# Kernel optimization log

Measured on AMD Instinct MI355X. Metric: run time of the kernel, lower is better.

The kernel has to match this reference:

```python
import jax, jax.numpy as jnp
import numpy as np

COUNT_PRIOR_LOG_ODDS = -2.0  # frozen value of exponential_decay(**cfg.OBJ_PRES_COUNT_LOG_PRIOR)
EPS = 1e-9                   # safe_log epsilon
B, H, W = 1024, 16, 16


def setup_inputs() -> dict:
    key = jax.random.key(0)
    k1, k2 = jax.random.split(key)
    z_pres = jax.random.uniform(k1, (B, 1, H, W), dtype=jnp.float32)
    z_pres_prob = jax.random.uniform(k2, (B, 1, H, W), dtype=jnp.float32)
    return {"z_pres": z_pres, "z_pres_prob": z_pres_prob}


def _safe_log(x):
    return jnp.log(x + EPS)


def reference(z_pres, z_pres_prob):
    b, _, h, w = z_pres.shape
    hw = h * w
    s = hw + 1  # count support size

    count_support = jnp.arange(s, dtype=jnp.float32)  # [S]
    p = 1.0 / (jnp.exp(jnp.float32(-COUNT_PRIOR_LOG_ODDS)) + 1.0)
    cd0 = (1.0 - p) * p ** count_support
    cd0 = cd0 / cd0.sum()
    cd0 = jnp.broadcast_to(cd0[None, :], (b, s))      # count_distribution [B, S]
    csf0 = jnp.zeros((b, 1), jnp.float32)             # count_so_far [B, 1]

    # flatten grid in row-major (h, w) order to scan axis: [HW, B, 1]
    probs = z_pres_prob.reshape(b, 1, hw).transpose(2, 0, 1)
    pres = z_pres.reshape(b, 1, hw).transpose(2, 0, 1)
    steps = jnp.arange(hw, dtype=jnp.float32)

    def step(carry, xs):
        cd, csf = carry                 # [B, S], [B, 1]
        prob, zp, i = xs                # [B, 1], [B, 1], scalar
        denom = hw - i
        # P(z=1 | C, z_prev): clamp(count_support - count_so_far, 0, HW - i) / (HW - i)
        p_z_given = jnp.clip(count_support[None, :] - csf, 0.0, denom) / denom  # [B, S]
        p_z = jnp.sum(cd * p_z_given, axis=1, keepdims=True)                    # [B, 1] (the bmm)
        kl = (prob * (_safe_log(prob) - _safe_log(p_z))
              + (1.0 - prob) * (_safe_log(1.0 - prob) - _safe_log(1.0 - p_z)))
        sample = jnp.round(zp)                                                  # [B, 1]
        mult = sample * p_z_given + (1.0 - sample) * (1.0 - p_z_given)          # [B, S]
        cd1 = mult * cd
        norm = jnp.clip(jnp.sum(cd1, axis=1, keepdims=True), 1e-6, None)
        return (cd1 / norm, csf + sample), kl

    (_, _), kls = jax.lax.scan(step, (cd0, csf0), (probs, pres, steps))
    # kls: [HW, B, 1] -> obj_kl [B, 1, H, W]
    return kls.transpose(1, 2, 0).reshape(b, 1, h, w)
```

## Files before the change

kernel.cpp:

```cpp
#include <hip/hip_runtime.h>
#include <math.h>

#define HW 256
#define MINNORM 1.17549435e-38f


template <int CTRL>
__device__ __forceinline__ float dpp_sra(float x) {
    int s = __builtin_amdgcn_update_dpp(0, __builtin_bit_cast(int, x),
                                        CTRL, 0xf, 0xf, true);
    return x + __builtin_bit_cast(float, s);
}

__device__ __forceinline__ float rdlane(float x, int l) {
    return __builtin_bit_cast(float,
        __builtin_amdgcn_readlane(__builtin_bit_cast(int, x), l));
}

__device__ __forceinline__ void wave_total2(float x, float y,
                                            float& sx, float& sy) {
    x = dpp_sra<0x111>(x);  y = dpp_sra<0x111>(y);
    x = dpp_sra<0x112>(x);  y = dpp_sra<0x112>(y);
    x = dpp_sra<0x114>(x);  y = dpp_sra<0x114>(y);
    x = dpp_sra<0x118>(x);  y = dpp_sra<0x118>(y);
    const float a0 = rdlane(x, 15), b0 = rdlane(y, 15);
    const float a1 = rdlane(x, 31), b1 = rdlane(y, 31);
    const float a2 = rdlane(x, 47), b2 = rdlane(y, 47);
    sx = (a0 + a1) + a2;
    sy = (b0 + b1) + b2;
}

__global__ void __launch_bounds__(64, 1)
spair_count_kl(const float* __restrict__ z_pres,
               const float* __restrict__ z_prob,
               float* __restrict__ out) {
    float tok;
    asm volatile("s_setreg_imm32_b32 hwreg(HW_REG_MODE, 4, 2), 0\n\t"
                 "v_mov_b32 %0, 0" : "=v"(tok));

    const int lane = threadIdx.x;
    const int b = blockIdx.x;

    const float e2f = (float)exp(2.0);
    const float pf  = (float)(1.0 / ((double)e2f + 1.0));
    const double pd = (double)pf;
    const double l2p = log2(pd);
    float cd = 0.0f;
    if (lane <= 41) {
        const double powj = exp2((double)lane * l2p);
        float v = (float)((1.0 - pd) * powj);
        cd = (v < MINNORM) ? 0.0f : v;
    }
    {
        float s = cd;
#pragma unroll
        for (int off = 32; off > 0; off >>= 1) s += __shfl_xor(s, off, 64);
        cd = cd / s;
    }
    cd += tok;
    const float jf = (float)lane;
    float csf = tok;

    const float it0 = 1.0f / (float)(HW - lane);
    const float it1 = 1.0f / (float)(HW - 64 - lane);
    const float it2 = 1.0f / (float)(HW - 128 - lane);
    const float it3 = 1.0f / (float)(HW - 192 - lane);

    const float* presb = z_pres + (size_t)b * HW;
    const float* probb = z_prob + (size_t)b * HW;
    float* outb = out + (size_t)b * HW;

    bool dead = false;

#pragma unroll 1
    for (int k = 0; k < 4; ++k) {
        const float myprob = probb[k * 64 + lane];
        const float mypres = presb[k * 64 + lane];
        const unsigned long long smask = __ballot(rintf(mypres) != 0.0f);
        float my_pz = 0.0f;
        const float itk = (k == 0) ? it0 : (k == 1) ? it1 : (k == 2) ? it2 : it3;

        if (!dead) {
#pragma unroll 1
            for (int blk = 0; blk < 4; ++blk) {
                float p2 = 1.0f;
#pragma unroll
                for (int u = 0; u < 16; ++u) {
                    const int ii = blk * 16 + u;
                    const int i = k * 64 + ii;
                    const float fden = (float)(HW - i);
                    const float inv = rdlane(itk, ii);
                    const bool s1 = ((smask >> ii) & 1ULL) != 0ULL;

                    const float t = fminf(fmaxf(jf - csf, 0.0f), fden);
                    const float pg = (t == fden) ? 1.0f : t * inv;
                    const float mult = s1 ? pg : (1.0f - pg);

                    const float prodm = cd * mult;
                    const float p1 = cd * pg;
                    float p1s;
                    wave_total2(prodm, p1, p2, p1s);
                    const float norm = fmaxf(p2, 1e-6f);
                    const float invn = __builtin_amdgcn_rcpf(norm);
                    cd = prodm * invn;
                    csf += s1 ? 1.0f : 0.0f;

                    const float pz = s1 ? p2 : p1s;
                    my_pz = (ii == lane) ? pz : my_pz;
                }
                if (p2 == 0.0f) { dead = true; break; }
            }
        }

        const float prob = myprob;
        const float pz = my_pz;
        const float kl = prob * (logf(prob + 1e-9f) - logf(pz + 1e-9f))
                       + (1.0f - prob) * (logf((1.0f - prob) + 1e-9f)
                                        - logf((1.0f - pz) + 1e-9f));
        outb[k * 64 + lane] = kl;
    }
}

extern "C" void kernel_launch(void* const* d_in, const int* in_sizes, int n_in,
                              void* d_out, int out_size, void* d_ws, size_t ws_size,
                              hipStream_t stream) {
    const float* z_pres = (const float*)d_in[0];
    const float* z_prob = (const float*)d_in[1];
    float* out = (float*)d_out;
    const int nbatch = in_sizes[0] / HW;
    spair_count_kl<<<dim3(nbatch), dim3(64), 0, stream>>>(z_pres, z_prob, out);
}
```

Baseline: 69.35 us.

## Fuse two scan steps per wave reduction round to halve serial reductions

Processes scan steps in pairs. The second step's unnormalised distribution is computed from the first's, and all four sums (two norms, two p_z values) go through two wave_total2 calls, so each pair needs one reduction round on the serial critical path instead of two. The FP mode now keeps denormals, and the code flushes values below the smallest normal by explicit compares to reproduce the old flush-to-zero behaviour. It adds extra multiplies, compares and reciprocals per pair, and the deferred normalisation risks small numeric differences.

```diff
diff --git a/kernel.cpp b/kernel.cpp
--- a/kernel.cpp
+++ b/kernel.cpp
@@ -35,7 +35,7 @@
                const float* __restrict__ z_prob,
                float* __restrict__ out) {
     float tok;
-    asm volatile("s_setreg_imm32_b32 hwreg(HW_REG_MODE, 4, 2), 0\n\t"
+    asm volatile("s_setreg_imm32_b32 hwreg(HW_REG_MODE, 4, 2), 3\n\t"
                  "v_mov_b32 %0, 0" : "=v"(tok));
 
     const int lane = threadIdx.x;
@@ -83,32 +83,55 @@
         if (!dead) {
 #pragma unroll 1
             for (int blk = 0; blk < 4; ++blk) {
-                float p2 = 1.0f;
+                float sent = 1.0f;
 #pragma unroll
-                for (int u = 0; u < 16; ++u) {
-                    const int ii = blk * 16 + u;
-                    const int i = k * 64 + ii;
-                    const float fden = (float)(HW - i);
-                    const float inv = rdlane(itk, ii);
-                    const bool s1 = ((smask >> ii) & 1ULL) != 0ULL;
+                for (int pr = 0; pr < 8; ++pr) {
+                    const int ii0 = blk * 16 + pr * 2, ii1 = ii0 + 1;
+                    const int i0 = k * 64 + ii0;
+                    const float fden0 = (float)(HW - i0);
+                    const float fden1 = (float)(HW - i0 - 1);
+                    const float inv0 = rdlane(itk, ii0);
+                    const float inv1 = rdlane(itk, ii1);
+                    const bool s0 = ((smask >> ii0) & 1ULL) != 0ULL;
+                    const bool s1b = ((smask >> ii1) & 1ULL) != 0ULL;
 
-                    const float t = fminf(fmaxf(jf - csf, 0.0f), fden);
-                    const float pg = (t == fden) ? 1.0f : t * inv;
-                    const float mult = s1 ? pg : (1.0f - pg);
+                    const float t0 = fminf(fmaxf(jf - csf, 0.0f), fden0);
+                    const float pg0 = (t0 == fden0) ? 1.0f : t0 * inv0;
+                    const float mult0 = s0 ? pg0 : (1.0f - pg0);
+                    const float csfA = csf + (s0 ? 1.0f : 0.0f);
+                    const float tA = fminf(fmaxf(jf - csfA, 0.0f), fden1);
+                    const float pg1 = (tA == fden1) ? 1.0f : tA * inv1;
+                    const float mult1 = s1b ? pg1 : (1.0f - pg1);
 
-                    const float prodm = cd * mult;
-                    const float p1 = cd * pg;
-                    float p1s;
-                    wave_total2(prodm, p1, p2, p1s);
-                    const float norm = fmaxf(p2, 1e-6f);
-                    const float invn = __builtin_amdgcn_rcpf(norm);
-                    cd = prodm * invn;
-                    csf += s1 ? 1.0f : 0.0f;
+                    const float a_raw = cd * mult0;
+                    const float af = (a_raw < MINNORM) ? 0.0f : a_raw;
+                    const float b_raw = af * mult1;
 
-                    const float pz = s1 ? p2 : p1s;
-                    my_pz = (ii == lane) ? pz : my_pz;
+                    const float z0t = cd * pg0;
+                    const float z1t = af * pg1;
+
+                    float n0, n1raw, z0, z1;
+                    wave_total2(af, b_raw, n0, n1raw);
+                    wave_total2(z0t, z1t, z0, z1);
+
+                    const float norm0 = fmaxf(n0, 1e-6f);
+                    const float invn0 = __builtin_amdgcn_rcpf(norm0);
+                    const float q = b_raw * invn0;
+                    const float qf = (q < MINNORM) ? 0.0f : q;
+                    const float norm1 = fmaxf(n1raw * invn0, 1e-6f);
+                    const float invn1 = __builtin_amdgcn_rcpf(norm1);
+                    const float cdn = qf * invn1;
+                    cd = (cdn < MINNORM) ? 0.0f : cdn;
+                    csf = csfA + (s1b ? 1.0f : 0.0f);
+
+                    const float pz0 = z0;
+                    const float pz1 = z1 * invn0;
+                    my_pz = (ii0 == lane) ? pz0 : my_pz;
+                    my_pz = (ii1 == lane) ? pz1 : my_pz;
+
+                    sent = n1raw;
                 }
-                if (p2 == 0.0f) { dead = true; break; }
+                if (sent == 0.0f) { dead = true; break; }
             }
         }
 
```

Measured after the change: 69.52 us. Within noise of the previous version (+0.2%).
